# Optimization experiments

Hardware: AMD Instinct MI355X
Metric: run time of the kernel (lower is better)

Reference implementation:

```python
import jax, jax.numpy as jnp
import numpy as np

N = 50000   # full-order mesh size
n = 10      # latent dim
MU = 32     # neighbourhood / window size
B = 8       # batch of snapshots


def setup_inputs() -> dict:
    key = jax.random.key(0)
    ks = jax.random.split(key, 6)
    x = jax.random.normal(ks[0], (B, N), jnp.float32)
    enc_w = jax.random.normal(ks[1], (n, N), jnp.float32) * 0.01  # torch Linear weight [n, N]
    enc_b = jax.random.normal(ks[2], (n,), jnp.float32) * 0.01
    decoder = jax.random.uniform(ks[3], (n, N), jnp.float32, minval=-0.01, maxval=0.01)
    bandwidth_layers = jax.random.uniform(ks[4], (n, n, N), jnp.float32, minval=-0.01, maxval=0.01)
    neighbours = jax.random.randint(ks[5], (N, MU), 0, N, jnp.int32)
    return dict(x=x, enc_w=enc_w, enc_b=enc_b, decoder=decoder,
                bandwidth_layers=bandwidth_layers, neighbours=neighbours)


def reference(x, enc_w, enc_b, decoder, bandwidth_layers, neighbours):
    mu = neighbours.shape[1]
    # encode: torch Linear -> x @ W.T + b                      [B, n]
    encoded = x @ enc_w.T + enc_b
    # bandwidths: bmm(encoded.repeat(n,1,1), bw).permute(1,0,2) -> sigmoid   [B, n, N]
    w = jax.nn.sigmoid(jnp.einsum('bk,ikp->bip', encoded, bandwidth_layers))
    # bubble window per scalar w: relu(1 - x^2/(w*mu)^2), normalized over mu  [B, n, N, mu]
    xs2 = (jnp.arange(mu, dtype=x.dtype) ** 2)  # [mu]
    win = jax.nn.relu(1.0 - xs2 / (w[..., None] * mu) ** 2)
    win = win / jnp.sum(win, axis=-1, keepdims=True)
    # gather decoder rows at each node's neighbours            [n, N, mu]
    gathered = jnp.take(decoder, neighbours, axis=1)
    # smooth_vec: sum over neighbourhood                       [B, n, N]
    smoothed = jnp.einsum('ipm,bipm->bip', gathered, win)
    # final bmm: encoded [B,1,n] @ smoothed [B,n,N] -> [B,N]
    return jnp.einsum('bi,bip->bp', encoded, smoothed)
```

## Files before the change

kernel.cpp:

```cpp
#include <hip/hip_runtime.h>
#include <hip/hip_bf16.h>

#define N_NODES 50000
#define NLAT 10
#define MU 32
#define BATCH 8
#define CHUNK 2000
#define NCHUNK 25
#define ENC_BLOCKS (BATCH * NLAT * NCHUNK)
#define TR_BLOCKS ((N_NODES + 255) / 256)
#define DT_STRIDE 16
#define NPB 32
#define SG_MSTRIDE 388

__global__ __launch_bounds__(256) void encode_a_transpose(
    const float* __restrict__ x, const float* __restrict__ enc_w,
    const float* __restrict__ dec,
    float* __restrict__ partial, float* __restrict__ dec_t) {
    const int bid = blockIdx.x;
    if (bid < ENC_BLOCKS) {
        const int c  = bid % NCHUNK;
        const int bi = bid / NCHUNK;
        const int b = bi / NLAT, i = bi % NLAT;
        const float4* xr = (const float4*)(x + (size_t)b * N_NODES + c * CHUNK);
        const float4* wr = (const float4*)(enc_w + (size_t)i * N_NODES + c * CHUNK);
        float part = 0.0f;
        for (int q = threadIdx.x; q < CHUNK / 4; q += 256) {
            float4 xv = xr[q], wv = wr[q];
            part += xv.x * wv.x + xv.y * wv.y + xv.z * wv.z + xv.w * wv.w;
        }
        for (int off = 32; off; off >>= 1) part += __shfl_down(part, off, 64);
        __shared__ float s[4];
        if ((threadIdx.x & 63) == 0) s[threadIdx.x >> 6] = part;
        __syncthreads();
        if (threadIdx.x == 0) partial[bid] = (s[0] + s[1]) + (s[2] + s[3]);
    } else {
        const int p = (bid - ENC_BLOCKS) * 256 + threadIdx.x;
        if (p >= N_NODES) return;
        float v[DT_STRIDE];
        #pragma unroll
        for (int i = 0; i < NLAT; ++i) v[i] = dec[(size_t)i * N_NODES + p];
        #pragma unroll
        for (int i = NLAT; i < DT_STRIDE; ++i) v[i] = 0.0f;
        float4* dst = (float4*)(dec_t + (size_t)p * DT_STRIDE);
        #pragma unroll
        for (int q = 0; q < 4; ++q)
            dst[q] = make_float4(v[4*q], v[4*q+1], v[4*q+2], v[4*q+3]);
    }
}

__global__ __launch_bounds__(128) void encode_stage_b(
    const float* __restrict__ partial, const float* __restrict__ enc_b,
    float* __restrict__ enc) {
    const int t = threadIdx.x;
    if (t < BATCH * NLAT) {
        float s = 0.0f;
        #pragma unroll
        for (int c = 0; c < NCHUNK; ++c) s += partial[t * NCHUNK + c];
        enc[t] = s + enc_b[t % NLAT];
    }
}

__global__ __launch_bounds__(256) void nrbs_main_kernel(
    const float* __restrict__ dec_t,
    const float* __restrict__ bw,
    const int*   __restrict__ nbr,
    const float* __restrict__ enc,
    float*       __restrict__ out) {
    __shared__ float s_enc[BATCH * NLAT];
    __shared__ float s_g[MU * SG_MSTRIDE];
    const int tid = threadIdx.x;
    if (tid < BATCH * NLAT) s_enc[tid] = enc[tid];
    __syncthreads();

    const int b  = tid & 7;
    const int nl = tid >> 3;
    const int p  = blockIdx.x * NPB + nl;
    const bool act = (p < N_NODES);

    float inv[NLAT];
    float tmax = 0.0f;
    if (act) {
        const float* bwp = bw + p;
        #pragma unroll
        for (int i = 0; i < NLAT; ++i) {
            float z = 0.0f;
            #pragma unroll
            for (int k = 0; k < NLAT; ++k)
                z = fmaf(s_enc[b * NLAT + k],
                         bwp[(size_t)(i * NLAT + k) * N_NODES], z);
            const float w = 1.0f / (1.0f + __expf(-z));
            const float t = w * (float)MU;
            tmax = fmaxf(tmax, t);
            inv[i] = 1.0f / (t * t);
        }
    }
    float tm = tmax;
    tm = fmaxf(tm, __shfl_xor(tm, 1, 64));
    tm = fmaxf(tm, __shfl_xor(tm, 2, 64));
    tm = fmaxf(tm, __shfl_xor(tm, 4, 64));
    const int mcap = min(MU, (int)tm + 1);

    if (act) {
        #pragma unroll
        for (int j = 0; j < 4; ++j) {
            const int m = b + 8 * j;
            if (m < mcap) {
                const int idx = nbr[(size_t)p * MU + m];
                const float4* gp = (const float4*)(dec_t + (size_t)idx * DT_STRIDE);
                const float4 g0 = gp[0], g1 = gp[1], g2 = gp[2];
                float4* dst = (float4*)(s_g + m * SG_MSTRIDE + nl * 12);
                dst[0] = g0; dst[1] = g1; dst[2] = g2;
            }
        }
    }
    __syncthreads();

    if (!act) return;

    float asum[NLAT], ssum[NLAT];
    #pragma unroll
    for (int i = 0; i < NLAT; ++i) { asum[i] = 0.0f; ssum[i] = 0.0f; }

    for (int m = 0; m < mcap; ++m) {
        const float m2 = (float)(m * m);
        const float* gr = s_g + m * SG_MSTRIDE + nl * 12;
        const float4 ga = *(const float4*)(gr);
        const float4 gb = *(const float4*)(gr + 4);
        const float2 gc = *(const float2*)(gr + 8);
        const float g[NLAT] = {ga.x, ga.y, ga.z, ga.w,
                               gb.x, gb.y, gb.z, gb.w, gc.x, gc.y};
        #pragma unroll
        for (int i = 0; i < NLAT; ++i) {
            const float win = fmaxf(0.0f, fmaf(-m2, inv[i], 1.0f));
            ssum[i] += win;
            asum[i] = fmaf(g[i], win, asum[i]);
        }
    }

    float acc = 0.0f;
    #pragma unroll
    for (int i = 0; i < NLAT; ++i)
        acc = fmaf(s_enc[b * NLAT + i], asum[i] / ssum[i], acc);
    out[(size_t)b * N_NODES + p] = acc;
}

extern "C" void kernel_launch(void* const* d_in, const int* in_sizes, int n_in,
                              void* d_out, int out_size, void* d_ws, size_t ws_size,
                              hipStream_t stream) {
    const float* x       = (const float*)d_in[0];
    const float* enc_w   = (const float*)d_in[1];
    const float* enc_b   = (const float*)d_in[2];
    const float* decoder = (const float*)d_in[3];
    const float* bwl     = (const float*)d_in[4];
    const int*   nbr     = (const int*)d_in[5];
    float* out = (float*)d_out;

    float* enc     = (float*)d_ws;
    float* partial = (float*)((char*)d_ws + 1024);
    float* dec_t   = (float*)((char*)d_ws + 65536);

    encode_a_transpose<<<ENC_BLOCKS + TR_BLOCKS, 256, 0, stream>>>(
        x, enc_w, decoder, partial, dec_t);
    encode_stage_b<<<1, 128, 0, stream>>>(partial, enc_b, enc);

    const int blocks = (N_NODES + NPB - 1) / NPB;
    nrbs_main_kernel<<<blocks, 256, 0, stream>>>(dec_t, bwl, nbr, enc, out);
}
```

Before: 113.9 us.

## Fuse encode reduction into main kernel and restructure bandwidth and gather phases

Drops the separate encode_stage_b launch: each main-kernel block re-reduces the encode partials itself. Bandwidth sigmoid evaluation is reorganised so each bw row is loaded once per node and reused across all batch entries, with the results held in shared memory. The neighbour gather no longer stages through shared memory: each thread reads neighbour indices as int4 and loads the decoder rows directly. Blocks grow to 512 threads covering 64 nodes. The trade-off is redundant partial reductions in every block, a shared-memory atomicMax, and uncoalesced direct gathers in the inner loop.

```diff
diff --git a/kernel.cpp b/kernel.cpp
--- a/kernel.cpp
+++ b/kernel.cpp
@@ -10,8 +10,8 @@
 #define ENC_BLOCKS (BATCH * NLAT * NCHUNK)
 #define TR_BLOCKS ((N_NODES + 255) / 256)
 #define DT_STRIDE 16
-#define NPB 32
-#define SG_MSTRIDE 388
+#define NPB 64
+#define INV_STRIDE (NPB + 2)
 
 __global__ __launch_bounds__(256) void encode_a_transpose(
     const float* __restrict__ x, const float* __restrict__ enc_w,
@@ -49,92 +49,90 @@
     }
 }
 
-__global__ __launch_bounds__(128) void encode_stage_b(
-    const float* __restrict__ partial, const float* __restrict__ enc_b,
-    float* __restrict__ enc) {
-    const int t = threadIdx.x;
-    if (t < BATCH * NLAT) {
-        float s = 0.0f;
-        #pragma unroll
-        for (int c = 0; c < NCHUNK; ++c) s += partial[t * NCHUNK + c];
-        enc[t] = s + enc_b[t % NLAT];
-    }
-}
-
-__global__ __launch_bounds__(256) void nrbs_main_kernel(
+__global__ __launch_bounds__(512) void nrbs_main_kernel(
     const float* __restrict__ dec_t,
     const float* __restrict__ bw,
     const int*   __restrict__ nbr,
-    const float* __restrict__ enc,
+    const float* __restrict__ partial,
+    const float* __restrict__ enc_b,
     float*       __restrict__ out) {
     __shared__ float s_enc[BATCH * NLAT];
-    __shared__ float s_g[MU * SG_MSTRIDE];
+    __shared__ float s_inv[BATCH * NLAT * INV_STRIDE];
+    __shared__ int   s_tm[NPB];
     const int tid = threadIdx.x;
-    if (tid < BATCH * NLAT) s_enc[tid] = enc[tid];
+
+    if (tid < BATCH * NLAT) {
+        float s = 0.0f;
+        #pragma unroll
+        for (int c = 0; c < NCHUNK; ++c) s += partial[tid * NCHUNK + c];
+        s_enc[tid] = s + enc_b[tid % NLAT];
+    }
+    if (tid < NPB) s_tm[tid] = 0;
+    __syncthreads();
+
+    {
+        const int g    = tid >> 6;
+        const int lane = tid & 63;
+        const int p    = blockIdx.x * NPB + lane;
+        if (p < N_NODES) {
+            float tloc = 0.0f;
+            for (int i = g; i < NLAT; i += 8) {
+                float bwv[NLAT];
+                #pragma unroll
+                for (int k = 0; k < NLAT; ++k)
+                    bwv[k] = bw[((size_t)(i * NLAT + k)) * N_NODES + p];
+                #pragma unroll
+                for (int b = 0; b < BATCH; ++b) {
+                    float z = 0.0f;
+                    #pragma unroll
+                    for (int k = 0; k < NLAT; ++k)
+                        z = fmaf(s_enc[b * NLAT + k], bwv[k], z);
+                    const float w = 1.0f / (1.0f + __expf(-z));
+                    const float t = w * (float)MU;
+                    tloc = fmaxf(tloc, t);
+                    s_inv[(b * NLAT + i) * INV_STRIDE + lane] = 1.0f / (t * t);
+                }
+            }
+            atomicMax(&s_tm[lane], __float_as_int(tloc));
+        }
+    }
     __syncthreads();
 
     const int b  = tid & 7;
     const int nl = tid >> 3;
     const int p  = blockIdx.x * NPB + nl;
-    const bool act = (p < N_NODES);
+    if (p >= N_NODES) return;
+
+    const int mcap = min(MU, (int)__int_as_float(s_tm[nl]) + 1);
 
     float inv[NLAT];
-    float tmax = 0.0f;
-    if (act) {
-        const float* bwp = bw + p;
-        #pragma unroll
-        for (int i = 0; i < NLAT; ++i) {
-            float z = 0.0f;
-            #pragma unroll
-            for (int k = 0; k < NLAT; ++k)
-                z = fmaf(s_enc[b * NLAT + k],
-                         bwp[(size_t)(i * NLAT + k) * N_NODES], z);
-            const float w = 1.0f / (1.0f + __expf(-z));
-            const float t = w * (float)MU;
-            tmax = fmaxf(tmax, t);
-            inv[i] = 1.0f / (t * t);
-        }
-    }
-    float tm = tmax;
-    tm = fmaxf(tm, __shfl_xor(tm, 1, 64));
-    tm = fmaxf(tm, __shfl_xor(tm, 2, 64));
-    tm = fmaxf(tm, __shfl_xor(tm, 4, 64));
-    const int mcap = min(MU, (int)tm + 1);
-
-    if (act) {
-        #pragma unroll
-        for (int j = 0; j < 4; ++j) {
-            const int m = b + 8 * j;
-            if (m < mcap) {
-                const int idx = nbr[(size_t)p * MU + m];
-                const float4* gp = (const float4*)(dec_t + (size_t)idx * DT_STRIDE);
-                const float4 g0 = gp[0], g1 = gp[1], g2 = gp[2];
-                float4* dst = (float4*)(s_g + m * SG_MSTRIDE + nl * 12);
-                dst[0] = g0; dst[1] = g1; dst[2] = g2;
-            }
-        }
-    }
-    __syncthreads();
-
-    if (!act) return;
+    #pragma unroll
+    for (int i = 0; i < NLAT; ++i)
+        inv[i] = s_inv[(b * NLAT + i) * INV_STRIDE + nl];
 
     float asum[NLAT], ssum[NLAT];
     #pragma unroll
     for (int i = 0; i < NLAT; ++i) { asum[i] = 0.0f; ssum[i] = 0.0f; }
 
-    for (int m = 0; m < mcap; ++m) {
-        const float m2 = (float)(m * m);
-        const float* gr = s_g + m * SG_MSTRIDE + nl * 12;
-        const float4 ga = *(const float4*)(gr);
-        const float4 gb = *(const float4*)(gr + 4);
-        const float2 gc = *(const float2*)(gr + 8);
-        const float g[NLAT] = {ga.x, ga.y, ga.z, ga.w,
-                               gb.x, gb.y, gb.z, gb.w, gc.x, gc.y};
+    const int4* nb4 = (const int4*)(nbr + (size_t)p * MU);
+    for (int q = 0; 4 * q < mcap; ++q) {
+        const int4 v = nb4[q];
+        const int idx[4] = {v.x, v.y, v.z, v.w};
         #pragma unroll
-        for (int i = 0; i < NLAT; ++i) {
-            const float win = fmaxf(0.0f, fmaf(-m2, inv[i], 1.0f));
-            ssum[i] += win;
-            asum[i] = fmaf(g[i], win, asum[i]);
+        for (int j = 0; j < 4; ++j) {
+            const int m = 4 * q + j;
+            const float m2 = (float)(m * m);
+            const float4* gp = (const float4*)(dec_t + (size_t)idx[j] * DT_STRIDE);
+            const float4 g0 = gp[0], g1 = gp[1];
+            const float2 g2 = *(const float2*)(&gp[2]);
+            const float g[NLAT] = {g0.x, g0.y, g0.z, g0.w,
+                                   g1.x, g1.y, g1.z, g1.w, g2.x, g2.y};
+            #pragma unroll
+            for (int i = 0; i < NLAT; ++i) {
+                const float win = fmaxf(0.0f, fmaf(-m2, inv[i], 1.0f));
+                ssum[i] += win;
+                asum[i] = fmaf(g[i], win, asum[i]);
+            }
         }
     }
 
@@ -156,14 +154,13 @@
     const int*   nbr     = (const int*)d_in[5];
     float* out = (float*)d_out;
 
-    float* enc     = (float*)d_ws;
     float* partial = (float*)((char*)d_ws + 1024);
     float* dec_t   = (float*)((char*)d_ws + 65536);
 
     encode_a_transpose<<<ENC_BLOCKS + TR_BLOCKS, 256, 0, stream>>>(
         x, enc_w, decoder, partial, dec_t);
-    encode_stage_b<<<1, 128, 0, stream>>>(partial, enc_b, enc);
 
     const int blocks = (N_NODES + NPB - 1) / NPB;
-    nrbs_main_kernel<<<blocks, 256, 0, stream>>>(dec_t, bwl, nbr, enc, out);
+    nrbs_main_kernel<<<blocks, 512, 0, stream>>>(
+        dec_t, bwl, nbr, partial, enc_b, out);
 }
```

Result: faster. 110.7 us (-2.8%).
